# Optimization experiments

Hardware: AMD Instinct MI355X
Metric: run time of the kernel (lower is better)

## Reference

```python
import jax, jax.numpy as jnp
import numpy as np

B, C, T = 32, 64, 8192
OUT, K = 129, 32
TWO_PI = 2.0 * np.pi
DROP_THRESH = 0.1  # squared-distance threshold for channel dropping


def setup_inputs() -> dict:
    key = jax.random.key(0)
    k1, k2, k3, k4, k5 = jax.random.split(key, 5)
    X = jax.random.normal(k1, (B, C, T), dtype=jnp.float32)
    positions = jax.random.uniform(k2, (B, C, 2), dtype=jnp.float32)
    drop_idx = jax.random.randint(k3, (B,), 0, C)
    scale = 1.0 / (K * K)
    z_real = jax.random.normal(k4, (OUT, K * K), dtype=jnp.float32) * scale
    z_imag = jax.random.normal(k5, (OUT, K * K), dtype=jnp.float32) * scale
    return {"X": X, "positions": positions, "drop_idx": drop_idx,
            "z_real": z_real, "z_imag": z_imag}


def reference(X, positions, drop_idx, z_real, z_imag):
    # frequency grid: feature index f = l_idx*K + k_idx (row-major over [l, k])
    kk = jnp.arange(1, K + 1, dtype=jnp.float32)
    coef_k = jnp.tile(kk, K)            # [K*K] varies fastest
    coef_l = jnp.repeat(kk, K)          # [K*K]

    x = positions[..., 0]               # [B, C]
    y = positions[..., 1]
    # phase: [B, C, K*K]
    phase = TWO_PI * (x[..., None] * coef_k + y[..., None] * coef_l)
    cos_mat = jnp.cos(phase)
    sin_mat = jnp.sin(phase)

    # a: [B, OUT, C]
    a = (jnp.einsum('of,bcf->boc', z_real, cos_mat)
         + jnp.einsum('of,bcf->boc', z_imag, sin_mat))

    # channel drop: remove all channels within sqdist < 0.1 of the dropped electrode
    pd = positions[jnp.arange(B), drop_idx]                 # [B, 2]
    dist = jnp.sum((positions - pd[:, None, :]) ** 2, axis=-1)  # [B, C]
    keep = dist >= DROP_THRESH                              # [B, C]

    a = jnp.where(keep[:, None, :], a, -1e9)
    attn = jax.nn.softmax(a, axis=2)                        # [B, OUT, C]
    # out: [B, OUT, T]
    return jnp.einsum('boc,bct->bot', attn, X)
```

## Files before the change

kernel.cpp:

```cpp
#include <hip/hip_runtime.h>
#include <math.h>

typedef __bf16 bf16x8 __attribute__((ext_vector_type(8)));
typedef unsigned short u16x8 __attribute__((ext_vector_type(8)));
typedef float f32x4 __attribute__((ext_vector_type(4)));

namespace {
constexpr int kB   = 32;
constexpr int kC   = 64;
constexpr int kT   = 8192;
constexpr int kOUT = 129;
constexpr int kKK  = 1024;
constexpr int kNFC = 16;
constexpr int kFCH = 64;
}

__device__ inline float sin2pi(float r) {
  float o; asm("v_sin_f32 %0, %1" : "=v"(o) : "v"(r)); return o;
}
__device__ inline float cos2pi(float r) {
  float o; asm("v_cos_f32 %0, %1" : "=v"(o) : "v"(r)); return o;
}
__device__ inline unsigned short f2bf_rne(float f) {
  unsigned int u = __builtin_bit_cast(unsigned int, f);
  return (unsigned short)((u + 0x7fffu + ((u >> 16) & 1u)) >> 16);
}
__device__ inline float bf2f(unsigned short h) {
  return __builtin_bit_cast(float, (unsigned int)h << 16);
}

__global__ __launch_bounds__(512) void sa_phase_dot(
    const float* __restrict__ positions,
    const float* __restrict__ z_real,
    const float* __restrict__ z_imag,
    unsigned short* __restrict__ part)
{
  __shared__ float4 s_zr[kOUT * 16];
  __shared__ float4 s_zi[kOUT * 16];

  const int b   = blockIdx.x >> 4;
  const int fc  = blockIdx.x & 15;
  const int tid = threadIdx.x;

  const float4* zr4 = reinterpret_cast<const float4*>(z_real);
  const float4* zi4 = reinterpret_cast<const float4*>(z_imag);
  for (int i = tid; i < kOUT * 16; i += 512) {
    const int o = i >> 4, q = i & 15;
    s_zr[i] = zr4[o * (kKK / 4) + fc * 16 + q];
    s_zi[i] = zi4[o * (kKK / 4) + fc * 16 + q];
  }

  const int og = tid >> 6;
  const int c  = tid & 63;
  const float2 p = reinterpret_cast<const float2*>(positions)[b * kC + c];
  const float x = p.x, y = p.y;

  __syncthreads();

  float acc[17];
#pragma unroll
  for (int j = 0; j < 17; ++j) acc[j] = 0.f;

  const float lbase = (float)(fc * 2 + 1);
  for (int q4 = 0; q4 < 16; ++q4) {
    float cs[4], sn[4];
#pragma unroll
    for (int i = 0; i < 4; ++i) {
      const int ff = q4 * 4 + i;
      const float kf = (float)((ff & 31) + 1);
      const float lf = lbase + (float)(ff >> 5);
      const float w = __fadd_rn(__fmul_rn(x, kf), __fmul_rn(y, lf));
      const float r = w - floorf(w);
      sn[i] = sin2pi(r);
      cs[i] = cos2pi(r);
    }
#pragma unroll
    for (int j = 0; j < 17; ++j) {
      const int o = og + 8 * j;
      if (o < kOUT) {
        const float4 zr = s_zr[o * 16 + q4];
        const float4 zi = s_zi[o * 16 + q4];
        float a = acc[j];
        a = fmaf(zr.x, cs[0], a); a = fmaf(zi.x, sn[0], a);
        a = fmaf(zr.y, cs[1], a); a = fmaf(zi.y, sn[1], a);
        a = fmaf(zr.z, cs[2], a); a = fmaf(zi.z, sn[2], a);
        a = fmaf(zr.w, cs[3], a); a = fmaf(zi.w, sn[3], a);
        acc[j] = a;
      }
    }
  }

#pragma unroll
  for (int j = 0; j < 17; ++j) {
    const int o = og + 8 * j;
    if (o < kOUT)
      part[(((size_t)fc * kB + b) * kOUT + o) * kC + c] = f2bf_rne(acc[j]);
  }
}

__global__ __launch_bounds__(64) void sa_softmax(
    const unsigned short* __restrict__ part,
    const float* __restrict__ positions,
    const int*   __restrict__ drop_idx,
    unsigned short* __restrict__ a_hi,
    unsigned short* __restrict__ a_lo)
{
  const int bo = blockIdx.x;
  const int b  = bo / kOUT;
  const int o  = bo - b * kOUT;
  const int c  = threadIdx.x;

  float a = 0.f;
#pragma unroll
  for (int fc = 0; fc < kNFC; ++fc)
    a += bf2f(part[(((size_t)fc * kB + b) * kOUT + o) * kC + c]);

  const float2 p  = reinterpret_cast<const float2*>(positions)[b * kC + c];
  const int    di = drop_idx[b];
  const float2 pd = reinterpret_cast<const float2*>(positions)[b * kC + di];
  const float dx = p.x - pd.x;
  const float dy = p.y - pd.y;
  const float d2 = __fadd_rn(__fmul_rn(dx, dx), __fmul_rn(dy, dy));
  if (d2 < 0.1f) a = -1e9f;

  float m = a;
#pragma unroll
  for (int off = 32; off; off >>= 1) m = fmaxf(m, __shfl_xor(m, off));
  const float e = expf(a - m);
  float s = e;
#pragma unroll
  for (int off = 32; off; off >>= 1) s += __shfl_xor(s, off);

  const float att = e / s;
  const unsigned short h = f2bf_rne(att);
  const float res = att - bf2f(h);
  a_hi[((size_t)b * kOUT + o) * kC + c] = h;
  a_lo[((size_t)b * kOUT + o) * kC + c] = f2bf_rne(res);
}

__global__ __launch_bounds__(256) void sa_apply_mfma(
    const float* __restrict__ X,
    const unsigned short* __restrict__ a_hi,
    const unsigned short* __restrict__ a_lo,
    float* __restrict__ out)
{
  __shared__ unsigned short s_a[2 * 144 * kC];

  const int b   = blockIdx.x >> 7;
  const int tc  = blockIdx.x & 127;
  const int t0  = tc * 64;
  const int tid = threadIdx.x;

  {
    char* sb = reinterpret_cast<char*>(s_a);
    for (int i = tid; i < 2 * 144 * 8; i += 256) {
      const int tile = (i >= 144 * 8) ? 1 : 0;
      const int r    = (i >> 3) - tile * 144;
      const int ch   = i & 7;
      float4 v;
      if (r < kOUT) {
        const unsigned short* src =
            (tile ? a_lo : a_hi) + ((size_t)b * kOUT + r) * kC + ch * 8;
        v = *reinterpret_cast<const float4*>(src);
      } else {
        v = make_float4(0.f, 0.f, 0.f, 0.f);
      }
      const int byte = tile * (144 * 128) + r * 128 + ((ch * 16) ^ ((r & 7) << 4));
      *reinterpret_cast<float4*>(sb + byte) = v;
    }
  }

  const int wave = tid >> 6;
  const int lane = tid & 63;
  const int t    = t0 + wave * 16 + (lane & 15);
  const int cg   = lane >> 4;

  const float* Xb = X + (size_t)b * kC * kT;
  float xv[16];
#pragma unroll
  for (int s2 = 0; s2 < 2; ++s2)
#pragma unroll
    for (int j = 0; j < 8; ++j)
      xv[s2 * 8 + j] = Xb[(size_t)(s2 * 32 + cg * 8 + j) * kT + t];

  u16x8 uh0, uh1, ul0, ul1;
#pragma unroll
  for (int j = 0; j < 8; ++j) {
    float f = xv[j];
    unsigned short h = f2bf_rne(f);
    uh0[j] = h; ul0[j] = f2bf_rne(f - bf2f(h));
    f = xv[8 + j];
    h = f2bf_rne(f);
    uh1[j] = h; ul1[j] = f2bf_rne(f - bf2f(h));
  }
  const bf16x8 Xh0 = __builtin_bit_cast(bf16x8, uh0);
  const bf16x8 Xh1 = __builtin_bit_cast(bf16x8, uh1);
  const bf16x8 Xl0 = __builtin_bit_cast(bf16x8, ul0);
  const bf16x8 Xl1 = __builtin_bit_cast(bf16x8, ul1);

  __syncthreads();

  const char* sb = reinterpret_cast<const char*>(s_a);
  float* outb = out + (size_t)b * kOUT * kT;

  for (int m = 0; m < 9; ++m) {
    const int row  = m * 16 + (lane & 15);
    const int base = row * 128;
    const int sw   = (row & 7) << 4;
    const int gb   = cg * 16;

    const bf16x8 Ah0 = *reinterpret_cast<const bf16x8*>(sb + base + ((gb     ) ^ sw));
    const bf16x8 Ah1 = *reinterpret_cast<const bf16x8*>(sb + base + ((gb + 64) ^ sw));
    const bf16x8 Al0 = *reinterpret_cast<const bf16x8*>(sb + 144 * 128 + base + ((gb     ) ^ sw));
    const bf16x8 Al1 = *reinterpret_cast<const bf16x8*>(sb + 144 * 128 + base + ((gb + 64) ^ sw));

    f32x4 acc = {0.f, 0.f, 0.f, 0.f};
    acc = __builtin_amdgcn_mfma_f32_16x16x32_bf16(Ah0, Xh0, acc, 0, 0, 0);
    acc = __builtin_amdgcn_mfma_f32_16x16x32_bf16(Ah1, Xh1, acc, 0, 0, 0);
    acc = __builtin_amdgcn_mfma_f32_16x16x32_bf16(Al0, Xh0, acc, 0, 0, 0);
    acc = __builtin_amdgcn_mfma_f32_16x16x32_bf16(Al1, Xh1, acc, 0, 0, 0);
    acc = __builtin_amdgcn_mfma_f32_16x16x32_bf16(Ah0, Xl0, acc, 0, 0, 0);
    acc = __builtin_amdgcn_mfma_f32_16x16x32_bf16(Ah1, Xl1, acc, 0, 0, 0);

#pragma unroll
    for (int r = 0; r < 4; ++r) {
      const int o = m * 16 + cg * 4 + r;
      if (o < kOUT) outb[(size_t)o * kT + t] = acc[r];
    }
  }
}

extern "C" void kernel_launch(void* const* d_in, const int* in_sizes, int n_in,
                              void* d_out, int out_size, void* d_ws, size_t ws_size,
                              hipStream_t stream) {
  (void)in_sizes; (void)n_in; (void)out_size; (void)ws_size;
  const float* X         = (const float*)d_in[0];
  const float* positions = (const float*)d_in[1];
  const int*   drop_idx  = (const int*)d_in[2];
  const float* z_real    = (const float*)d_in[3];
  const float* z_imag    = (const float*)d_in[4];
  float* out = (float*)d_out;

  unsigned short* part = (unsigned short*)d_ws;
  unsigned short* ahi  = part + (size_t)kNFC * kB * kOUT * kC;
  unsigned short* alo  = ahi + (size_t)kB * kOUT * kC;

  sa_phase_dot<<<kB * kNFC, 512, 0, stream>>>(positions, z_real, z_imag, part);
  sa_softmax<<<kB * kOUT, 64, 0, stream>>>(part, positions, drop_idx, ahi, alo);
  sa_apply_mfma<<<kB * 128, 256, 0, stream>>>(X, ahi, alo, out);
}
```

Measured before the change: 240.3 us.

## Move phase-dot to split-bf16 MFMA and double time tile in apply kernel

The scalar FMA phase-dot kernel is replaced by an MFMA kernel. It builds cos/sin operands in registers, splits both z and the trig values into hi/lo bf16 pairs, and writes fp32 partial sums over 8 frequency chunks instead of bf16 partials over 16. The apply kernel now handles 128 time steps per block, with two independent MFMA accumulator chains per wave. This halves the grid and reuses the staged attention tile across more outputs. The costs are more register pressure in both kernels and a larger fp32 partial buffer.

Result: slower. 247.0 us (+2.8%).

```diff
diff --git a/kernel.cpp b/kernel.cpp
--- a/kernel.cpp
+++ b/kernel.cpp
@@ -11,8 +11,7 @@
 constexpr int kT   = 8192;
 constexpr int kOUT = 129;
 constexpr int kKK  = 1024;
-constexpr int kNFC = 16;
-constexpr int kFCH = 64;
+constexpr int kNKC = 8;
 }
 
 __device__ inline float sin2pi(float r) {
@@ -28,78 +27,108 @@
 __device__ inline float bf2f(unsigned short h) {
   return __builtin_bit_cast(float, (unsigned int)h << 16);
 }
-
-__global__ __launch_bounds__(512) void sa_phase_dot(
+__device__ inline void split8(const float* v, bf16x8& hi, bf16x8& lo) {
+  u16x8 h, l;
+#pragma unroll
+  for (int j = 0; j < 8; ++j) {
+    const unsigned short hh = f2bf_rne(v[j]);
+    h[j] = hh;
+    l[j] = f2bf_rne(v[j] - bf2f(hh));
+  }
+  hi = __builtin_bit_cast(bf16x8, h);
+  lo = __builtin_bit_cast(bf16x8, l);
+}
+
+__global__ __launch_bounds__(256) void sa_phase_mfma(
     const float* __restrict__ positions,
     const float* __restrict__ z_real,
     const float* __restrict__ z_imag,
-    unsigned short* __restrict__ part)
+    float* __restrict__ part)
 {
-  __shared__ float4 s_zr[kOUT * 16];
-  __shared__ float4 s_zi[kOUT * 16];
-
-  const int b   = blockIdx.x >> 4;
-  const int fc  = blockIdx.x & 15;
-  const int tid = threadIdx.x;
-
-  const float4* zr4 = reinterpret_cast<const float4*>(z_real);
-  const float4* zi4 = reinterpret_cast<const float4*>(z_imag);
-  for (int i = tid; i < kOUT * 16; i += 512) {
-    const int o = i >> 4, q = i & 15;
-    s_zr[i] = zr4[o * (kKK / 4) + fc * 16 + q];
-    s_zi[i] = zi4[o * (kKK / 4) + fc * 16 + q];
-  }
-
-  const int og = tid >> 6;
-  const int c  = tid & 63;
+  const int bid = blockIdx.x;
+  const int b   = bid & 31;
+  const int kc  = (bid >> 5) & 7;
+  const int mh  = bid >> 8;
+  const int w    = threadIdx.x >> 6;
+  const int lane = threadIdx.x & 63;
+  const int cg   = lane >> 4;
+  const int cl   = lane & 15;
+  const int c    = w * 16 + cl;
+  const int f0   = kc * 128;
+
   const float2 p = reinterpret_cast<const float2*>(positions)[b * kC + c];
-  const float x = p.x, y = p.y;
-
-  __syncthreads();
-
-  float acc[17];
-#pragma unroll
-  for (int j = 0; j < 17; ++j) acc[j] = 0.f;
-
-  const float lbase = (float)(fc * 2 + 1);
-  for (int q4 = 0; q4 < 16; ++q4) {
-    float cs[4], sn[4];
-#pragma unroll
-    for (int i = 0; i < 4; ++i) {
-      const int ff = q4 * 4 + i;
-      const float kf = (float)((ff & 31) + 1);
-      const float lf = lbase + (float)(ff >> 5);
-      const float w = __fadd_rn(__fmul_rn(x, kf), __fmul_rn(y, lf));
-      const float r = w - floorf(w);
-      sn[i] = sin2pi(r);
-      cs[i] = cos2pi(r);
-    }
-#pragma unroll
-    for (int j = 0; j < 17; ++j) {
-      const int o = og + 8 * j;
-      if (o < kOUT) {
-        const float4 zr = s_zr[o * 16 + q4];
-        const float4 zi = s_zi[o * 16 + q4];
-        float a = acc[j];
-        a = fmaf(zr.x, cs[0], a); a = fmaf(zi.x, sn[0], a);
-        a = fmaf(zr.y, cs[1], a); a = fmaf(zi.y, sn[1], a);
-        a = fmaf(zr.z, cs[2], a); a = fmaf(zi.z, sn[2], a);
-        a = fmaf(zr.w, cs[3], a); a = fmaf(zi.w, sn[3], a);
-        acc[j] = a;
-      }
-    }
-  }
-
-#pragma unroll
-  for (int j = 0; j < 17; ++j) {
-    const int o = og + 8 * j;
-    if (o < kOUT)
-      part[(((size_t)fc * kB + b) * kOUT + o) * kC + c] = f2bf_rne(acc[j]);
+
+  bf16x8 BcH[4], BcL[4], BsH[4], BsL[4];
+#pragma unroll
+  for (int ks = 0; ks < 4; ++ks) {
+    float cs[8], sn[8];
+#pragma unroll
+    for (int j = 0; j < 8; ++j) {
+      const int f = f0 + ks * 32 + 8 * cg + j;
+      const float kf = (float)((f & 31) + 1);
+      const float lf = (float)((f >> 5) + 1);
+      const float wv = __fadd_rn(__fmul_rn(p.x, kf), __fmul_rn(p.y, lf));
+      const float r  = wv - floorf(wv);
+      cs[j] = cos2pi(r);
+      sn[j] = sin2pi(r);
+    }
+    split8(cs, BcH[ks], BcL[ks]);
+    split8(sn, BsH[ks], BsL[ks]);
+  }
+
+  const int nm  = mh ? 4 : 5;
+  const int ob0 = mh * 80;
+
+#pragma unroll
+  for (int m = 0; m < 5; ++m) {
+    if (m < nm) {
+      const int ob = ob0 + m * 16;
+      const int oa = ob + cl;
+      bf16x8 ArH[4], ArL[4], AiH[4], AiL[4];
+      if (oa < kOUT) {
+        const float* zr = z_real + (size_t)oa * kKK + f0 + 8 * cg;
+        const float* zi = z_imag + (size_t)oa * kKK + f0 + 8 * cg;
+#pragma unroll
+        for (int ks = 0; ks < 4; ++ks) {
+          float vr[8], vi[8];
+          *reinterpret_cast<float4*>(vr)     = *reinterpret_cast<const float4*>(zr + ks * 32);
+          *reinterpret_cast<float4*>(vr + 4) = *reinterpret_cast<const float4*>(zr + ks * 32 + 4);
+          *reinterpret_cast<float4*>(vi)     = *reinterpret_cast<const float4*>(zi + ks * 32);
+          *reinterpret_cast<float4*>(vi + 4) = *reinterpret_cast<const float4*>(zi + ks * 32 + 4);
+          split8(vr, ArH[ks], ArL[ks]);
+          split8(vi, AiH[ks], AiL[ks]);
+        }
+      } else {
+#pragma unroll
+        for (int ks = 0; ks < 4; ++ks) {
+          u16x8 z0 = {0,0,0,0,0,0,0,0};
+          ArH[ks] = ArL[ks] = AiH[ks] = AiL[ks] = __builtin_bit_cast(bf16x8, z0);
+        }
+      }
+
+      f32x4 acc = {0.f, 0.f, 0.f, 0.f};
+#pragma unroll
+      for (int ks = 0; ks < 4; ++ks) {
+        acc = __builtin_amdgcn_mfma_f32_16x16x32_bf16(ArH[ks], BcH[ks], acc, 0, 0, 0);
+        acc = __builtin_amdgcn_mfma_f32_16x16x32_bf16(ArH[ks], BcL[ks], acc, 0, 0, 0);
+        acc = __builtin_amdgcn_mfma_f32_16x16x32_bf16(ArL[ks], BcH[ks], acc, 0, 0, 0);
+        acc = __builtin_amdgcn_mfma_f32_16x16x32_bf16(AiH[ks], BsH[ks], acc, 0, 0, 0);
+        acc = __builtin_amdgcn_mfma_f32_16x16x32_bf16(AiH[ks], BsL[ks], acc, 0, 0, 0);
+        acc = __builtin_amdgcn_mfma_f32_16x16x32_bf16(AiL[ks], BsH[ks], acc, 0, 0, 0);
+      }
+
+#pragma unroll
+      for (int r = 0; r < 4; ++r) {
+        const int o = ob + cg * 4 + r;
+        if (o < kOUT)
+          part[(((size_t)kc * kB + b) * kOUT + o) * kC + c] = acc[r];
+      }
+    }
   }
 }
 
 __global__ __launch_bounds__(64) void sa_softmax(
-    const unsigned short* __restrict__ part,
+    const float* __restrict__ part,
     const float* __restrict__ positions,
     const int*   __restrict__ drop_idx,
     unsigned short* __restrict__ a_hi,
@@ -112,8 +141,8 @@
 
   float a = 0.f;
 #pragma unroll
-  for (int fc = 0; fc < kNFC; ++fc)
-    a += bf2f(part[(((size_t)fc * kB + b) * kOUT + o) * kC + c]);
+  for (int fc = 0; fc < kNKC; ++fc)
+    a += part[(((size_t)fc * kB + b) * kOUT + o) * kC + c];
 
   const float2 p  = reinterpret_cast<const float2*>(positions)[b * kC + c];
   const int    di = drop_idx[b];
@@ -146,9 +175,9 @@
 {
   __shared__ unsigned short s_a[2 * 144 * kC];
 
-  const int b   = blockIdx.x >> 7;
-  const int tc  = blockIdx.x & 127;
-  const int t0  = tc * 64;
+  const int b   = blockIdx.x >> 6;
+  const int tc  = blockIdx.x & 63;
+  const int t0  = tc * 128;
   const int tid = threadIdx.x;
 
   {
@@ -172,31 +201,27 @@
 
   const int wave = tid >> 6;
   const int lane = tid & 63;
-  const int t    = t0 + wave * 16 + (lane & 15);
+  const int cl   = lane & 15;
   const int cg   = lane >> 4;
+  const int tA   = t0 + wave * 32 + cl;
+  const int tB   = tA + 16;
 
   const float* Xb = X + (size_t)b * kC * kT;
-  float xv[16];
+  float xvA[16], xvB[16];
 #pragma unroll
   for (int s2 = 0; s2 < 2; ++s2)
 #pragma unroll
-    for (int j = 0; j < 8; ++j)
-      xv[s2 * 8 + j] = Xb[(size_t)(s2 * 32 + cg * 8 + j) * kT + t];
-
-  u16x8 uh0, uh1, ul0, ul1;
-#pragma unroll
-  for (int j = 0; j < 8; ++j) {
-    float f = xv[j];
-    unsigned short h = f2bf_rne(f);
-    uh0[j] = h; ul0[j] = f2bf_rne(f - bf2f(h));
-    f = xv[8 + j];
-    h = f2bf_rne(f);
-    uh1[j] = h; ul1[j] = f2bf_rne(f - bf2f(h));
-  }
-  const bf16x8 Xh0 = __builtin_bit_cast(bf16x8, uh0);
-  const bf16x8 Xh1 = __builtin_bit_cast(bf16x8, uh1);
-  const bf16x8 Xl0 = __builtin_bit_cast(bf16x8, ul0);
-  const bf16x8 Xl1 = __builtin_bit_cast(bf16x8, ul1);
+    for (int j = 0; j < 8; ++j) {
+      const size_t row = (size_t)(s2 * 32 + cg * 8 + j) * kT;
+      xvA[s2 * 8 + j] = Xb[row + tA];
+      xvB[s2 * 8 + j] = Xb[row + tB];
+    }
+
+  bf16x8 XhA0, XlA0, XhA1, XlA1, XhB0, XlB0, XhB1, XlB1;
+  split8(xvA,     XhA0, XlA0);
+  split8(xvA + 8, XhA1, XlA1);
+  split8(xvB,     XhB0, XlB0);
+  split8(xvB + 8, XhB1, XlB1);
 
   __syncthreads();
 
@@ -204,7 +229,7 @@
   float* outb = out + (size_t)b * kOUT * kT;
 
   for (int m = 0; m < 9; ++m) {
-    const int row  = m * 16 + (lane & 15);
+    const int row  = m * 16 + cl;
     const int base = row * 128;
     const int sw   = (row & 7) << 4;
     const int gb   = cg * 16;
@@ -214,18 +239,28 @@
     const bf16x8 Al0 = *reinterpret_cast<const bf16x8*>(sb + 144 * 128 + base + ((gb     ) ^ sw));
     const bf16x8 Al1 = *reinterpret_cast<const bf16x8*>(sb + 144 * 128 + base + ((gb + 64) ^ sw));
 
-    f32x4 acc = {0.f, 0.f, 0.f, 0.f};
-    acc = __builtin_amdgcn_mfma_f32_16x16x32_bf16(Ah0, Xh0, acc, 0, 0, 0);
-    acc = __builtin_amdgcn_mfma_f32_16x16x32_bf16(Ah1, Xh1, acc, 0, 0, 0);
-    acc = __builtin_amdgcn_mfma_f32_16x16x32_bf16(Al0, Xh0, acc, 0, 0, 0);
-    acc = __builtin_amdgcn_mfma_f32_16x16x32_bf16(Al1, Xh1, acc, 0, 0, 0);
-    acc = __builtin_amdgcn_mfma_f32_16x16x32_bf16(Ah0, Xl0, acc, 0, 0, 0);
-    acc = __builtin_amdgcn_mfma_f32_16x16x32_bf16(Ah1, Xl1, acc, 0, 0, 0);
+    f32x4 accA = {0.f, 0.f, 0.f, 0.f};
+    f32x4 accB = {0.f, 0.f, 0.f, 0.f};
+    accA = __builtin_amdgcn_mfma_f32_16x16x32_bf16(Ah0, XhA0, accA, 0, 0, 0);
+    accB = __builtin_amdgcn_mfma_f32_16x16x32_bf16(Ah0, XhB0, accB, 0, 0, 0);
+    accA = __builtin_amdgcn_mfma_f32_16x16x32_bf16(Ah1, XhA1, accA, 0, 0, 0);
+    accB = __builtin_amdgcn_mfma_f32_16x16x32_bf16(Ah1, XhB1, accB, 0, 0, 0);
+    accA = __builtin_amdgcn_mfma_f32_16x16x32_bf16(Al0, XhA0, accA, 0, 0, 0);
+    accB = __builtin_amdgcn_mfma_f32_16x16x32_bf16(Al0, XhB0, accB, 0, 0, 0);
+    accA = __builtin_amdgcn_mfma_f32_16x16x32_bf16(Al1, XhA1, accA, 0, 0, 0);
+    accB = __builtin_amdgcn_mfma_f32_16x16x32_bf16(Al1, XhB1, accB, 0, 0, 0);
+    accA = __builtin_amdgcn_mfma_f32_16x16x32_bf16(Ah0, XlA0, accA, 0, 0, 0);
+    accB = __builtin_amdgcn_mfma_f32_16x16x32_bf16(Ah0, XlB0, accB, 0, 0, 0);
+    accA = __builtin_amdgcn_mfma_f32_16x16x32_bf16(Ah1, XlA1, accA, 0, 0, 0);
+    accB = __builtin_amdgcn_mfma_f32_16x16x32_bf16(Ah1, XlB1, accB, 0, 0, 0);
 
 #pragma unroll
     for (int r = 0; r < 4; ++r) {
       const int o = m * 16 + cg * 4 + r;
-      if (o < kOUT) outb[(size_t)o * kT + t] = acc[r];
+      if (o < kOUT) {
+        outb[(size_t)o * kT + tA] = accA[r];
+        outb[(size_t)o * kT + tB] = accB[r];
+      }
     }
   }
 }
@@ -241,11 +276,11 @@
   const float* z_imag    = (const float*)d_in[4];
   float* out = (float*)d_out;
 
-  unsigned short* part = (unsigned short*)d_ws;
-  unsigned short* ahi  = part + (size_t)kNFC * kB * kOUT * kC;
-  unsigned short* alo  = ahi + (size_t)kB * kOUT * kC;
-
-  sa_phase_dot<<<kB * kNFC, 512, 0, stream>>>(positions, z_real, z_imag, part);
+  float* part = (float*)d_ws;
+  unsigned short* ahi = (unsigned short*)(part + (size_t)kNKC * kB * kOUT * kC);
+  unsigned short* alo = ahi + (size_t)kB * kOUT * kC;
+
+  sa_phase_mfma<<<kB * kNKC * 2, 256, 0, stream>>>(positions, z_real, z_imag, part);
   sa_softmax<<<kB * kOUT, 64, 0, stream>>>(part, positions, drop_idx, ahi, alo);
-  sa_apply_mfma<<<kB * 128, 256, 0, stream>>>(X, ahi, alo, out);
-}
+  sa_apply_mfma<<<kB * 64, 256, 0, stream>>>(X, ahi, alo, out);
+}
```
